# Performance work log

Hardware: AMD Instinct MI355X
Metric: run time of the kernel (lower is better)

## Reference

```python
import jax, jax.numpy as jnp
import numpy as np

C_M, C_Z, H, C_HID = 256, 128, 8, 32
N_SEQ, N_RES = 64, 384
INF = 1e9
EPS = 1e-5


def layernorm(x, w, b):
    mu = jnp.mean(x, axis=-1, keepdims=True)
    var = jnp.mean(jnp.square(x - mu), axis=-1, keepdims=True)
    return (x - mu) * jax.lax.rsqrt(var + EPS) * w + b


def setup_inputs() -> dict:
    key = jax.random.key(0)
    ks = jax.random.split(key, 6)
    m = jax.random.normal(ks[0], (N_SEQ, N_RES, C_M), dtype=jnp.float32)
    z = jax.random.normal(ks[1], (N_RES, N_RES, C_Z), dtype=jnp.float32)
    mask = jnp.ones((N_SEQ, N_RES), dtype=jnp.float32)
    return {
        "m": m,
        "z": z,
        "mask": mask,
        "ln_m_w": jnp.ones((C_M,), jnp.float32),
        "ln_m_b": jnp.zeros((C_M,), jnp.float32),
        "ln_z_w": jnp.ones((C_Z,), jnp.float32),
        "ln_z_b": jnp.zeros((C_Z,), jnp.float32),
        "W_z": jax.random.normal(ks[2], (C_Z, H), jnp.float32) * 0.05,
        "W_v": jax.random.normal(ks[3], (C_M, H * C_HID), jnp.float32) * 0.05,
        "W_g": jax.random.normal(ks[4], (C_M, H * C_HID), jnp.float32) * 0.05,
        "W_o": jax.random.normal(ks[5], (H * C_HID, C_M), jnp.float32) * 0.05,
    }


def reference(m, z, mask, ln_m_w, ln_m_b, ln_z_w, ln_z_b, W_z, W_v, W_g, W_o):
    S, N = m.shape[0], m.shape[1]
    # mask: max over MSA rows, keepdim -> [1, N]; bias -> [1,1,1,N]
    mask_max = jnp.max(mask, axis=-2, keepdims=True)
    mask_bias = (INF * (mask_max - 1.0))[:, None, None, :]  # [1,1,1,N]
    # pair bias: LN(z) @ W_z -> [N,N,H] -> [H,N,N]
    zb = layernorm(z, ln_z_w, ln_z_b) @ W_z  # [N,N,H]
    zb = jnp.transpose(zb, (2, 0, 1))  # [H,N,N]
    # LN on m
    m_ln = layernorm(m, ln_m_w, ln_m_b)  # [S,N,C_m]
    # values: [S,N,H*c] -> [S,H,N,c]
    v = (m_ln @ W_v).reshape(S, N, H, C_HID).transpose(0, 2, 1, 3)
    # attention weights from summed biases (no QK): [1,H,N,N] after broadcast
    a = jax.nn.softmax(mask_bias + zb[None], axis=-1)  # [1,H,N,N]
    # o = a @ v  -> [S,H,N,c]
    o = jnp.einsum('hqk,shkc->shqc', a[0], v)
    o = o.transpose(0, 2, 1, 3)  # [S,N,H,c]
    # sigmoid gate
    g = jax.nn.sigmoid(m_ln @ W_g).reshape(S, N, H, C_HID)
    o = (o * g).reshape(S, N, H * C_HID)
    return o @ W_o  # [S,N,C_m]
```

## Files before the change

### kernel.cpp

```cpp
#include <hip/hip_runtime.h>
#include <math.h>

#define S 64
#define NRES 384
#define CM 256
#define CZ 128
#define NH 8
#define CH 32
#define HC 256
#define NROW 147456

typedef unsigned short u16;
typedef __attribute__((ext_vector_type(8))) short bf16x8;
typedef __attribute__((ext_vector_type(4))) float f32x4;
typedef __attribute__((ext_vector_type(8))) unsigned short ushort8;
typedef __attribute__((ext_vector_type(4))) unsigned short ushort4_t;

#define OFF_BIAS 0
#define OFF_WT   200704
#define OFF_WOT  462848
#define OFF_A    593920
#define OFF_VT   2953216
#define OFF_G    15536128
#define OFF_O    28119040
#define OFF_MLN  40701952
#define OFF_ZB   OFF_O

__device__ __forceinline__ u16 f2bf(float f) {
    union { float f; unsigned int u; } v; v.f = f;
    unsigned int u = v.u;
    u += 0x7fff + ((u >> 16) & 1);
    return (u16)(u >> 16);
}
__device__ __forceinline__ float bf2f(u16 b) {
    union { float f; unsigned int u; } v; v.u = ((unsigned int)b) << 16;
    return v.f;
}
__device__ __forceinline__ void gload16(const u16* g, u16* l) {
    __builtin_amdgcn_global_load_lds(
        (const __attribute__((address_space(1))) void*)g,
        (__attribute__((address_space(3))) void*)l, 16, 0, 0);
}

__global__ __launch_bounds__(256) void k_stage1(
        const float* __restrict__ z, const float* __restrict__ Wz,
        const float* __restrict__ lzw, const float* __restrict__ lzb,
        const float* __restrict__ mask,
        const float* __restrict__ Wv, const float* __restrict__ Wg,
        const float* __restrict__ Wo, const float* __restrict__ m,
        const float* __restrict__ lmw, const float* __restrict__ lmb,
        float* __restrict__ zb, float* __restrict__ bias,
        u16* __restrict__ Wt, u16* __restrict__ Wot, u16* __restrict__ mln) {
    const int bid = blockIdx.x, tid = threadIdx.x;
    if (bid < 1152) {
        __shared__ u16 sWWT[16 * 128];
        __shared__ float sPart[2][2][8];
        const int wave = tid >> 6, lane = tid & 63;
        const int rl = lane & 15, kg = lane >> 4;
        if (tid < 128) {
            const int c = tid;
            const float4 wz0 = *(const float4*)&Wz[c * 8];
            const float4 wz1 = *(const float4*)&Wz[c * 8 + 4];
            const float lw = lzw[c], lbv = lzb[c];
            float wzv[8] = {wz0.x, wz0.y, wz0.z, wz0.w, wz1.x, wz1.y, wz1.z, wz1.w};
            float ww[8], wb[8];
            #pragma unroll
            for (int h = 0; h < 8; ++h) {
                ww[h] = lw * wzv[h];
                wb[h] = lbv * wzv[h];
                sWWT[h * 128 + c] = f2bf(ww[h]);
                sWWT[(8 + h) * 128 + c] = 0;
            }
            #pragma unroll
            for (int h = 0; h < 8; ++h) {
                #pragma unroll
                for (int off = 1; off < 64; off <<= 1) {
                    ww[h] += __shfl_xor(ww[h], off);
                    wb[h] += __shfl_xor(wb[h], off);
                }
            }
            if (lane == 0) {
                #pragma unroll
                for (int h = 0; h < 8; ++h) {
                    sPart[wave][0][h] = ww[h];
                    sPart[wave][1][h] = wb[h];
                }
            }
        }
        __syncthreads();
        const float c1 = (rl < 8) ? (sPart[0][0][rl] + sPart[1][0][rl]) : 0.f;
        const float c2 = (rl < 8) ? (sPart[0][1][rl] + sPart[1][1][rl]) : 0.f;
        bf16x8 bfr[4];
        #pragma unroll
        for (int t = 0; t < 4; ++t)
            bfr[t] = *(const bf16x8*)&sWWT[rl * 128 + kg * 8 + t * 32];
        #pragma unroll
        for (int it = 0; it < 2; ++it) {
            const int row0 = bid * 128 + it * 64 + wave * 16;
            const float* zrow = z + (size_t)(row0 + rl) * CZ + kg * 8;
            bf16x8 af[4];
            float sm = 0.f, sq = 0.f;
            #pragma unroll
            for (int t = 0; t < 4; ++t) {
                const float4 x0 = *(const float4*)&zrow[t * 32];
                const float4 x1 = *(const float4*)&zrow[t * 32 + 4];
                float xs[8] = {x0.x, x0.y, x0.z, x0.w, x1.x, x1.y, x1.z, x1.w};
                u16 tmp[8];
                #pragma unroll
                for (int e = 0; e < 8; ++e) {
                    sm += xs[e]; sq += xs[e] * xs[e];
                    tmp[e] = f2bf(xs[e]);
                }
                af[t] = *(bf16x8*)tmp;
            }
            sm += __shfl_xor(sm, 16); sq += __shfl_xor(sq, 16);
            sm += __shfl_xor(sm, 32); sq += __shfl_xor(sq, 32);
            const float mu = sm * (1.0f / CZ);
            const float var = sq * (1.0f / CZ) - mu * mu;
            const float rs = rsqrtf(var + 1e-5f);
            f32x4 acc = {};
            #pragma unroll
            for (int t = 0; t < 4; ++t)
                acc = __builtin_amdgcn_mfma_f32_16x16x32_bf16(af[t], bfr[t], acc, 0, 0, 0);
            f32x4 pv;
            #pragma unroll
            for (int r = 0; r < 4; ++r) {
                const int rr = kg * 4 + r;
                const float mu_r = __shfl(mu, rr);
                const float rs_r = __shfl(rs, rr);
                pv[r] = rs_r * (acc[r] - mu_r * c1) + c2;
            }
            if (rl < 8)
                *(f32x4*)&zb[(size_t)rl * NROW + row0 + kg * 4] = pv;
        }
    } else if (bid < 1154) {
        const int k = (bid - 1152) * 256 + tid;
        if (k < NRES) {
            float mx = -1e30f;
            for (int s = 0; s < S; ++s) mx = fmaxf(mx, mask[s * NRES + k]);
            bias[k] = 1e9f * (mx - 1.0f);
        }
    } else if (bid < 1666) {
        const int i = (bid - 1154) * 256 + tid;
        const int n = i >> 8, k = i & 255;
        const float v = (n < HC) ? Wv[(size_t)k * HC + n] : Wg[(size_t)k * HC + (n - HC)];
        Wt[i] = f2bf(v);
    } else if (bid < 1922) {
        const int i = (bid - 1666) * 256 + tid;
        const int n = i >> 8, k = i & 255;
        Wot[i] = f2bf(Wo[(size_t)k * CM + n]);
    } else {
        const int row = (bid - 1922) * 4 + (tid >> 6);
        const int lane = tid & 63;
        const float4 x = *(const float4*)&m[(size_t)row * CM + lane * 4];
        float sm = x.x + x.y + x.z + x.w;
        float sq = x.x*x.x + x.y*x.y + x.z*x.z + x.w*x.w;
        #pragma unroll
        for (int off = 32; off >= 1; off >>= 1) {
            sm += __shfl_xor(sm, off);
            sq += __shfl_xor(sq, off);
        }
        const float mu = sm * (1.0f / CM);
        const float var = sq * (1.0f / CM) - mu * mu;
        const float rs = rsqrtf(var + 1e-5f);
        const float4 w4 = *(const float4*)&lmw[lane * 4];
        const float4 b4 = *(const float4*)&lmb[lane * 4];
        u16 t4[4];
        t4[0] = f2bf((x.x - mu) * rs * w4.x + b4.x);
        t4[1] = f2bf((x.y - mu) * rs * w4.y + b4.y);
        t4[2] = f2bf((x.z - mu) * rs * w4.z + b4.z);
        t4[3] = f2bf((x.w - mu) * rs * w4.w + b4.w);
        *(ushort4_t*)&mln[(size_t)row * CM + lane * 4] = *(ushort4_t*)t4;
    }
}

__global__ __launch_bounds__(256) void k_stage2(
        const u16* __restrict__ mln, const u16* __restrict__ Wt,
        const float* __restrict__ zb, const float* __restrict__ bias,
        u16* __restrict__ vt, u16* __restrict__ g_, u16* __restrict__ a_out) {
    __shared__ u16 As[128][32];
    __shared__ u16 Bs[128][32];
    const int bid = blockIdx.x, tid = threadIdx.x;
    if (bid >= 768) {
        const int w = (bid - 768) * 4 + (tid >> 6);
        const int lane = tid & 63;
        const int h = w & 7, q = w >> 3;
        const float* zbh = zb + (size_t)h * NROW + (size_t)q * NRES;
        float v[6];
        float mx = -1e30f;
        #pragma unroll
        for (int t = 0; t < 6; ++t) {
            const int k = lane + 64 * t;
            v[t] = zbh[k] + bias[k];
            mx = fmaxf(mx, v[t]);
        }
        #pragma unroll
        for (int off = 32; off >= 1; off >>= 1) mx = fmaxf(mx, __shfl_xor(mx, off));
        float sum = 0.f;
        #pragma unroll
        for (int t = 0; t < 6; ++t) { v[t] = expf(v[t] - mx); sum += v[t]; }
        #pragma unroll
        for (int off = 32; off >= 1; off >>= 1) sum += __shfl_xor(sum, off);
        const float inv = 1.0f / sum;
        #pragma unroll
        for (int t = 0; t < 6; ++t)
            a_out[((size_t)h * NRES + q) * NRES + lane + 64 * t] = f2bf(v[t] * inv);
        return;
    }
    const int xcd = bid & 7, idx = bid >> 3;
    const int nt = idx & 3, mt = xcd * 24 + (idx >> 2);
    const int m0 = mt * 128, n0 = nt * 128;
    const int wave = tid >> 6, lane = tid & 63;
    const int wm = (wave >> 1) * 64, wn = (wave & 1) * 64;
    const int rl = lane & 15, kg = lane >> 4;
    const int lr = lane >> 2, lk = (lane & 3) * 8;
    const int wr = wave * 32;
    const u16* ag  = mln + (size_t)(m0 + wr + lr) * CM + lk;
    const u16* ag2 = ag + 16 * CM;
    const u16* bg  = Wt + (size_t)(n0 + wr + lr) * CM + lk;
    const u16* bg2 = bg + 16 * CM;
    u16* al  = &As[wr][0];
    u16* al2 = &As[wr + 16][0];
    u16* bl  = &Bs[wr][0];
    u16* bl2 = &Bs[wr + 16][0];
    const bool vhalf = (n0 < HC);
    f32x4 acc[4][4] = {};
    for (int kt = 0; kt < CM; kt += 32) {
        if (kt) __syncthreads();
        gload16(ag + kt, al);  gload16(ag2 + kt, al2);
        gload16(bg + kt, bl);  gload16(bg2 + kt, bl2);
        __syncthreads();
        bf16x8 af[4], bfr[4];
        #pragma unroll
        for (int i = 0; i < 4; ++i) af[i]  = *(const bf16x8*)&As[wm + i*16 + rl][kg*8];
        #pragma unroll
        for (int j = 0; j < 4; ++j) bfr[j] = *(const bf16x8*)&Bs[wn + j*16 + rl][kg*8];
        if (vhalf) {
            #pragma unroll
            for (int j = 0; j < 4; ++j)
                #pragma unroll
                for (int i = 0; i < 4; ++i)
                    acc[j][i] = __builtin_amdgcn_mfma_f32_16x16x32_bf16(bfr[j], af[i], acc[j][i], 0, 0, 0);
        } else {
            #pragma unroll
            for (int i = 0; i < 4; ++i)
                #pragma unroll
                for (int j = 0; j < 4; ++j)
                    acc[i][j] = __builtin_amdgcn_mfma_f32_16x16x32_bf16(af[i], bfr[j], acc[i][j], 0, 0, 0);
        }
    }
    if (vhalf) {
        #pragma unroll
        for (int j = 0; j < 4; ++j)
            #pragma unroll
            for (int r = 0; r < 4; ++r) {
                const int vcol = n0 + wn + j*16 + kg*4 + r;
                const int h = vcol >> 5, c = vcol & 31;
                #pragma unroll
                for (int i = 0; i < 4; ++i) {
                    const int mrowb = m0 + wm + i*16;
                    const int s = mrowb / NRES;
                    const int nn = mrowb - s * NRES + rl;
                    vt[(((size_t)h * S + s) * CH + c) * NRES + nn] = f2bf(acc[j][i][r]);
                }
            }
    } else {
        #pragma unroll
        for (int i = 0; i < 4; ++i)
            #pragma unroll
            for (int r = 0; r < 4; ++r) {
                const int row = m0 + wm + i*16 + kg*4 + r;
                #pragma unroll
                for (int j = 0; j < 4; ++j) {
                    const int gc = n0 + wn + j*16 + rl - HC;
                    g_[(size_t)row * HC + gc] = f2bf(1.0f / (1.0f + expf(-acc[i][j][r])));
                }
            }
    }
}

__global__ __launch_bounds__(256) void k_attn2(const u16* __restrict__ a_,
        const u16* __restrict__ vt, u16* __restrict__ o_) {
    __shared__ u16 As[128][32];
    __shared__ u16 Bs[128][32];
    const int tid = threadIdx.x;
    const int h = blockIdx.x & 7, rem = blockIdx.x >> 3;
    const int mt = rem >> 4, nt = rem & 15;
    const int q0 = mt * 128, sc0 = nt * 128;
    const int wave = tid >> 6, lane = tid & 63;
    const int wm = (wave >> 1) * 64, wn = (wave & 1) * 64;
    const int rl = lane & 15, kg = lane >> 4;
    const int lr = lane >> 2, lk = (lane & 3) * 8;
    const int wr = wave * 32;
    const u16* ag  = a_ + (size_t)h * NRES * NRES + (size_t)(q0 + wr + lr) * NRES + lk;
    const u16* ag2 = ag + 16 * NRES;
    const u16* bg  = vt + (size_t)h * S * CH * NRES + (size_t)(sc0 + wr + lr) * NRES + lk;
    const u16* bg2 = bg + 16 * NRES;
    u16* al  = &As[wr][0];
    u16* al2 = &As[wr + 16][0];
    u16* bl  = &Bs[wr][0];
    u16* bl2 = &Bs[wr + 16][0];
    f32x4 acc[4][4] = {};
    for (int kt = 0; kt < NRES; kt += 32) {
        if (kt) __syncthreads();
        gload16(ag + kt, al);  gload16(ag2 + kt, al2);
        gload16(bg + kt, bl);  gload16(bg2 + kt, bl2);
        __syncthreads();
        bf16x8 af[4], bfr[4];
        #pragma unroll
        for (int i = 0; i < 4; ++i) af[i]  = *(const bf16x8*)&As[wm + i*16 + rl][kg*8];
        #pragma unroll
        for (int j = 0; j < 4; ++j) bfr[j] = *(const bf16x8*)&Bs[wn + j*16 + rl][kg*8];
        #pragma unroll
        for (int i = 0; i < 4; ++i)
            #pragma unroll
            for (int j = 0; j < 4; ++j)
                acc[i][j] = __builtin_amdgcn_mfma_f32_16x16x32_bf16(af[i], bfr[j], acc[i][j], 0, 0, 0);
    }
    #pragma unroll
    for (int i = 0; i < 4; ++i)
        #pragma unroll
        for (int r = 0; r < 4; ++r) {
            const int q = q0 + wm + i*16 + kg*4 + r;
            #pragma unroll
            for (int j = 0; j < 4; ++j) {
                const int sc = sc0 + wn + j*16 + rl;
                const int s = sc >> 5, c = sc & 31;
                o_[(((size_t)s * NRES + q) * NH + h) * CH + c] = f2bf(acc[i][j][r]);
            }
        }
}

__global__ __launch_bounds__(256) void k_gemm_out(const u16* __restrict__ o_,
        const u16* __restrict__ g_, const u16* __restrict__ Wot,
        float* __restrict__ out) {
    __shared__ u16 As[128][40];
    __shared__ u16 Bs[128][32];
    const int tid = threadIdx.x;
    const int xcd = blockIdx.x & 7, idx = blockIdx.x >> 3;
    const int nt = idx & 1, mt = xcd * 24 + (idx >> 1);
    const int m0 = mt * 128, n0 = nt * 128;
    const int wave = tid >> 6, lane = tid & 63;
    const int wm = (wave >> 1) * 64, wn = (wave & 1) * 64;
    const int rl = lane & 15, kg = lane >> 4;
    const int lr = lane >> 2, lk = (lane & 3) * 8;
    const int wr = wave * 32;
    const int sr = tid >> 1, sh = (tid & 1) * 16;
    const u16* orow = o_ + (size_t)(m0 + sr) * HC;
    const u16* grow = g_ + (size_t)(m0 + sr) * HC;
    const u16* bg  = Wot + (size_t)(n0 + wr + lr) * HC + lk;
    const u16* bg2 = bg + 16 * HC;
    u16* bl  = &Bs[wr][0];
    u16* bl2 = &Bs[wr + 16][0];
    f32x4 acc[4][4] = {};
    for (int kt = 0; kt < HC; kt += 32) {
        if (kt) __syncthreads();
        gload16(bg + kt, bl);  gload16(bg2 + kt, bl2);
        {
            u16 tmp[16];
            const ushort8 ov0 = *(const ushort8*)&orow[kt + sh];
            const ushort8 ov1 = *(const ushort8*)&orow[kt + sh + 8];
            const ushort8 gv0 = *(const ushort8*)&grow[kt + sh];
            const ushort8 gv1 = *(const ushort8*)&grow[kt + sh + 8];
            #pragma unroll
            for (int p = 0; p < 8; ++p) {
                tmp[p]     = f2bf(bf2f(ov0[p]) * bf2f(gv0[p]));
                tmp[p + 8] = f2bf(bf2f(ov1[p]) * bf2f(gv1[p]));
            }
            *(ushort8*)&As[sr][sh]     = *(ushort8*)&tmp[0];
            *(ushort8*)&As[sr][sh + 8] = *(ushort8*)&tmp[8];
        }
        __syncthreads();
        bf16x8 af[4], bfr[4];
        #pragma unroll
        for (int i = 0; i < 4; ++i) af[i]  = *(const bf16x8*)&As[wm + i*16 + rl][kg*8];
        #pragma unroll
        for (int j = 0; j < 4; ++j) bfr[j] = *(const bf16x8*)&Bs[wn + j*16 + rl][kg*8];
        #pragma unroll
        for (int i = 0; i < 4; ++i)
            #pragma unroll
            for (int j = 0; j < 4; ++j)
                acc[i][j] = __builtin_amdgcn_mfma_f32_16x16x32_bf16(af[i], bfr[j], acc[i][j], 0, 0, 0);
    }
    #pragma unroll
    for (int i = 0; i < 4; ++i)
        #pragma unroll
        for (int r = 0; r < 4; ++r) {
            const int row = m0 + wm + i*16 + kg*4 + r;
            #pragma unroll
            for (int j = 0; j < 4; ++j)
                out[(size_t)row * CM + n0 + wn + j*16 + rl] = acc[i][j][r];
        }
}

extern "C" void kernel_launch(void* const* d_in, const int* in_sizes, int n_in,
                              void* d_out, int out_size, void* d_ws, size_t ws_size,
                              hipStream_t stream) {
    const float* m      = (const float*)d_in[0];
    const float* z      = (const float*)d_in[1];
    const float* mask   = (const float*)d_in[2];
    const float* ln_m_w = (const float*)d_in[3];
    const float* ln_m_b = (const float*)d_in[4];
    const float* ln_z_w = (const float*)d_in[5];
    const float* ln_z_b = (const float*)d_in[6];
    const float* Wz     = (const float*)d_in[7];
    const float* Wv     = (const float*)d_in[8];
    const float* Wg     = (const float*)d_in[9];
    const float* Wo     = (const float*)d_in[10];
    float* out = (float*)d_out;
    char* ws = (char*)d_ws;

    float* bias = (float*)(ws + OFF_BIAS);
    u16* Wt     = (u16*)(ws + OFF_WT);
    u16* Wot    = (u16*)(ws + OFF_WOT);
    u16* a      = (u16*)(ws + OFF_A);
    u16* vtw    = (u16*)(ws + OFF_VT);
    u16* gw     = (u16*)(ws + OFF_G);
    u16* ow     = (u16*)(ws + OFF_O);
    u16* mlnw   = (u16*)(ws + OFF_MLN);
    float* zbw  = (float*)(ws + OFF_ZB);

    k_stage1<<<8066, 256, 0, stream>>>(z, Wz, ln_z_w, ln_z_b, mask, Wv, Wg, Wo,
                                       m, ln_m_w, ln_m_b, zbw, bias, Wt, Wot, mlnw);
    k_stage2<<<1536, 256, 0, stream>>>(mlnw, Wt, zbw, bias, vtw, gw, a);
    k_attn2<<<384, 256, 0, stream>>>(a, vtw, ow);
    k_gemm_out<<<384, 256, 0, stream>>>(ow, gw, Wot, out);
}
```

Before: 76.77 us.

## Coalesce z loads, normalize before MFMA via swizzled LDS, drop softmax-invariant bias

Rewrites the pair-bias front stage so each wave loads 16 z rows with fully coalesced float4 reads, computes layernorm stats by shuffles, writes normalized bf16 into XOR-swizzled LDS and reads MFMA fragments from there. The ln_z bias contribution is dropped because a per-head constant cancels under the key-axis softmax, and the mean correction term is no longer needed. The mask max reduction is spread over four waves. Trades extra LDS traffic and more blocks for better global memory access on the dominant z read.

```diff
diff --git a/kernel.cpp b/kernel.cpp
--- a/kernel.cpp
+++ b/kernel.cpp
@@ -42,116 +42,113 @@
         (__attribute__((address_space(3))) void*)l, 16, 0, 0);
 }
 
-__global__ __launch_bounds__(256) void k_stage1(
+__global__ __launch_bounds__(256) void k_front(
         const float* __restrict__ z, const float* __restrict__ Wz,
-        const float* __restrict__ lzw, const float* __restrict__ lzb,
+        const float* __restrict__ lzw,
         const float* __restrict__ mask,
         const float* __restrict__ Wv, const float* __restrict__ Wg,
         const float* __restrict__ Wo, const float* __restrict__ m,
         const float* __restrict__ lmw, const float* __restrict__ lmb,
         float* __restrict__ zb, float* __restrict__ bias,
         u16* __restrict__ Wt, u16* __restrict__ Wot, u16* __restrict__ mln) {
+    __shared__ u16 SMEM[2048 + 4 * 2048];
     const int bid = blockIdx.x, tid = threadIdx.x;
-    if (bid < 1152) {
-        __shared__ u16 sWWT[16 * 128];
-        __shared__ float sPart[2][2][8];
-        const int wave = tid >> 6, lane = tid & 63;
-        const int rl = lane & 15, kg = lane >> 4;
+    const int wave = tid >> 6, lane = tid & 63;
+    const int rl = lane & 15, kg = lane >> 4;
+
+    if (bid < 2304) {
+        u16* sW  = SMEM;
+        u16* myZ = SMEM + 2048 + wave * 2048;
         if (tid < 128) {
             const int c = tid;
             const float4 wz0 = *(const float4*)&Wz[c * 8];
             const float4 wz1 = *(const float4*)&Wz[c * 8 + 4];
-            const float lw = lzw[c], lbv = lzb[c];
+            const float lw = lzw[c];
             float wzv[8] = {wz0.x, wz0.y, wz0.z, wz0.w, wz1.x, wz1.y, wz1.z, wz1.w};
-            float ww[8], wb[8];
             #pragma unroll
             for (int h = 0; h < 8; ++h) {
-                ww[h] = lw * wzv[h];
-                wb[h] = lbv * wzv[h];
-                sWWT[h * 128 + c] = f2bf(ww[h]);
-                sWWT[(8 + h) * 128 + c] = 0;
-            }
-            #pragma unroll
-            for (int h = 0; h < 8; ++h) {
-                #pragma unroll
-                for (int off = 1; off < 64; off <<= 1) {
-                    ww[h] += __shfl_xor(ww[h], off);
-                    wb[h] += __shfl_xor(wb[h], off);
-                }
-            }
-            if (lane == 0) {
-                #pragma unroll
-                for (int h = 0; h < 8; ++h) {
-                    sPart[wave][0][h] = ww[h];
-                    sPart[wave][1][h] = wb[h];
-                }
-            }
-        }
+                sW[h * 128 + c] = f2bf(lw * wzv[h]);
+                sW[(8 + h) * 128 + c] = 0;
+            }
+        }
+        const int row0 = bid * 64 + wave * 16;
+        const float4* zbase = (const float4*)(z + (size_t)row0 * CZ);
+        float4 xb[8];
+        #pragma unroll
+        for (int j = 0; j < 8; ++j) xb[j] = zbase[lane + 64 * j];
         __syncthreads();
-        const float c1 = (rl < 8) ? (sPart[0][0][rl] + sPart[1][0][rl]) : 0.f;
-        const float c2 = (rl < 8) ? (sPart[0][1][rl] + sPart[1][1][rl]) : 0.f;
         bf16x8 bfr[4];
         #pragma unroll
         for (int t = 0; t < 4; ++t)
-            bfr[t] = *(const bf16x8*)&sWWT[rl * 128 + kg * 8 + t * 32];
-        #pragma unroll
-        for (int it = 0; it < 2; ++it) {
-            const int row0 = bid * 128 + it * 64 + wave * 16;
-            const float* zrow = z + (size_t)(row0 + rl) * CZ + kg * 8;
-            bf16x8 af[4];
-            float sm = 0.f, sq = 0.f;
-            #pragma unroll
-            for (int t = 0; t < 4; ++t) {
-                const float4 x0 = *(const float4*)&zrow[t * 32];
-                const float4 x1 = *(const float4*)&zrow[t * 32 + 4];
-                float xs[8] = {x0.x, x0.y, x0.z, x0.w, x1.x, x1.y, x1.z, x1.w};
-                u16 tmp[8];
-                #pragma unroll
-                for (int e = 0; e < 8; ++e) {
-                    sm += xs[e]; sq += xs[e] * xs[e];
-                    tmp[e] = f2bf(xs[e]);
-                }
-                af[t] = *(bf16x8*)tmp;
-            }
-            sm += __shfl_xor(sm, 16); sq += __shfl_xor(sq, 16);
-            sm += __shfl_xor(sm, 32); sq += __shfl_xor(sq, 32);
-            const float mu = sm * (1.0f / CZ);
-            const float var = sq * (1.0f / CZ) - mu * mu;
+            bfr[t] = *(const bf16x8*)&sW[rl * 128 + t * 32 + kg * 8];
+        const int hw = lane >> 5, c4 = lane & 31;
+        float smj[8], sqj[8];
+        #pragma unroll
+        for (int j = 0; j < 8; ++j) {
+            const float4 x = xb[j];
+            smj[j] = x.x + x.y + x.z + x.w;
+            sqj[j] = x.x*x.x + x.y*x.y + x.z*x.z + x.w*x.w;
+        }
+        #pragma unroll
+        for (int j = 0; j < 8; ++j) {
+            #pragma unroll
+            for (int off = 1; off < 32; off <<= 1) {
+                smj[j] += __shfl_xor(smj[j], off);
+                sqj[j] += __shfl_xor(sqj[j], off);
+            }
+        }
+        #pragma unroll
+        for (int j = 0; j < 8; ++j) {
+            const int r = 2 * j + hw;
+            const float mu = smj[j] * (1.0f / CZ);
+            const float var = sqj[j] * (1.0f / CZ) - mu * mu;
             const float rs = rsqrtf(var + 1e-5f);
-            f32x4 acc = {};
-            #pragma unroll
-            for (int t = 0; t < 4; ++t)
-                acc = __builtin_amdgcn_mfma_f32_16x16x32_bf16(af[t], bfr[t], acc, 0, 0, 0);
-            f32x4 pv;
-            #pragma unroll
-            for (int r = 0; r < 4; ++r) {
-                const int rr = kg * 4 + r;
-                const float mu_r = __shfl(mu, rr);
-                const float rs_r = __shfl(rs, rr);
-                pv[r] = rs_r * (acc[r] - mu_r * c1) + c2;
-            }
-            if (rl < 8)
-                *(f32x4*)&zb[(size_t)rl * NROW + row0 + kg * 4] = pv;
-        }
-    } else if (bid < 1154) {
-        const int k = (bid - 1152) * 256 + tid;
-        if (k < NRES) {
-            float mx = -1e30f;
-            for (int s = 0; s < S; ++s) mx = fmaxf(mx, mask[s * NRES + k]);
+            const float4 x = xb[j];
+            u16 t4[4];
+            t4[0] = f2bf((x.x - mu) * rs);
+            t4[1] = f2bf((x.y - mu) * rs);
+            t4[2] = f2bf((x.z - mu) * rs);
+            t4[3] = f2bf((x.w - mu) * rs);
+            *(ushort4_t*)&myZ[r * 128 + ((c4 >> 1) ^ (r & 7)) * 8 + (c4 & 1) * 4] =
+                *(ushort4_t*)t4;
+        }
+        bf16x8 af[4];
+        #pragma unroll
+        for (int t = 0; t < 4; ++t)
+            af[t] = *(const bf16x8*)&myZ[rl * 128 + ((t * 4 + kg) ^ (rl & 7)) * 8];
+        f32x4 acc = {};
+        #pragma unroll
+        for (int t = 0; t < 4; ++t)
+            acc = __builtin_amdgcn_mfma_f32_16x16x32_bf16(af[t], bfr[t], acc, 0, 0, 0);
+        if (rl < 8)
+            *(f32x4*)&zb[(size_t)rl * NROW + row0 + kg * 4] = acc;
+    } else if (bid < 2310) {
+        float* sRed = (float*)SMEM;
+        const int k = (bid - 2304) * 64 + lane;
+        float mx = -1e30f;
+        #pragma unroll
+        for (int i = 0; i < 16; ++i) {
+            const int s = wave * 16 + i;
+            mx = fmaxf(mx, mask[(size_t)s * NRES + k]);
+        }
+        sRed[wave * 64 + lane] = mx;
+        __syncthreads();
+        if (wave == 0) {
+            mx = fmaxf(fmaxf(sRed[lane], sRed[64 + lane]),
+                       fmaxf(sRed[128 + lane], sRed[192 + lane]));
             bias[k] = 1e9f * (mx - 1.0f);
         }
-    } else if (bid < 1666) {
-        const int i = (bid - 1154) * 256 + tid;
+    } else if (bid < 2822) {
+        const int i = (bid - 2310) * 256 + tid;
         const int n = i >> 8, k = i & 255;
         const float v = (n < HC) ? Wv[(size_t)k * HC + n] : Wg[(size_t)k * HC + (n - HC)];
         Wt[i] = f2bf(v);
-    } else if (bid < 1922) {
-        const int i = (bid - 1666) * 256 + tid;
+    } else if (bid < 3078) {
+        const int i = (bid - 2822) * 256 + tid;
         const int n = i >> 8, k = i & 255;
         Wot[i] = f2bf(Wo[(size_t)k * CM + n]);
     } else {
-        const int row = (bid - 1922) * 4 + (tid >> 6);
-        const int lane = tid & 63;
+        const int row = (bid - 3078) * 4 + wave;
         const float4 x = *(const float4*)&m[(size_t)row * CM + lane * 4];
         float sm = x.x + x.y + x.z + x.w;
         float sq = x.x*x.x + x.y*x.y + x.z*x.z + x.w*x.w;
@@ -402,7 +399,6 @@
     const float* ln_m_w = (const float*)d_in[3];
     const float* ln_m_b = (const float*)d_in[4];
     const float* ln_z_w = (const float*)d_in[5];
-    const float* ln_z_b = (const float*)d_in[6];
     const float* Wz     = (const float*)d_in[7];
     const float* Wv     = (const float*)d_in[8];
     const float* Wg     = (const float*)d_in[9];
@@ -420,8 +416,8 @@
     u16* mlnw   = (u16*)(ws + OFF_MLN);
     float* zbw  = (float*)(ws + OFF_ZB);
 
-    k_stage1<<<8066, 256, 0, stream>>>(z, Wz, ln_z_w, ln_z_b, mask, Wv, Wg, Wo,
-                                       m, ln_m_w, ln_m_b, zbw, bias, Wt, Wot, mlnw);
+    k_front<<<9222, 256, 0, stream>>>(z, Wz, ln_z_w, mask, Wv, Wg, Wo, m,
+                                      ln_m_w, ln_m_b, zbw, bias, Wt, Wot, mlnw);
     k_stage2<<<1536, 256, 0, stream>>>(mlnw, Wt, zbw, bias, vtw, gw, a);
     k_attn2<<<384, 256, 0, stream>>>(a, vtw, ow);
     k_gemm_out<<<384, 256, 0, stream>>>(ow, gw, Wot, out);
```

Result: faster. 73.48 us (-4.3%).
